# Kernel tuning notes

Hardware: AMD Instinct MI355X
Metric: run time of the kernel (lower is better)

Reference implementation:

```python
import jax, jax.numpy as jnp
import numpy as np

B, N, E, DIN, DOUT = 8, 4096, 1024, 256, 256
EPS = 1e-8

def setup_inputs() -> dict:
    key = jax.random.key(0)
    k1, k2, k3, k4 = jax.random.split(key, 4)
    x = jax.random.normal(k1, (B, N, DIN), dtype=jnp.float32)
    H = jax.random.uniform(k2, (B, N, E), dtype=jnp.float32)
    weight = jax.random.normal(k3, (DIN, DOUT), dtype=jnp.float32) * (1.0 / np.sqrt(DOUT))
    bias = jax.random.normal(k4, (DOUT,), dtype=jnp.float32) * (1.0 / np.sqrt(DOUT))
    return {"x": x, "hypergraph_matrix": H, "weight": weight, "bias": bias}

def reference(x, hypergraph_matrix, weight, bias):
    H = hypergraph_matrix                      # [B, N, E]
    d_v = jnp.clip(jnp.sum(H, axis=2), EPS)    # node degrees [B, N]
    d_v_inv_sqrt = d_v ** -0.5
    d_e = jnp.clip(jnp.sum(H, axis=1), EPS)    # hyperedge degrees [B, E]
    d_e_inv = 1.0 / d_e
    # D_v^{-1/2} H D_e^{-1}
    step2 = d_v_inv_sqrt[:, :, None] * H * d_e_inv[:, None, :]   # [B, N, E]
    # (D_v^{-1/2} H D_e^{-1} H^T) D_v^{-1/2}  -- original materializes [B, N, N]
    step3 = jnp.einsum('bne,bme->bnm', step2, H)                 # [B, N, N]
    normalized_matrix = step3 * d_v_inv_sqrt[:, None, :]         # [B, N, N]
    support = jnp.einsum('bnd,df->bnf', x, weight)               # X Theta
    out = jnp.einsum('bnm,bmf->bnf', normalized_matrix, support) + bias
    # dropout is identity in eval / deterministic baseline
    return out
```

## Files before the change

### kernel.cpp

```cpp
#include <hip/hip_runtime.h>
#include <hip/hip_bf16.h>

#define BATCH 8
#define NN 4096
#define EE 1024
#define DIN 256
#define DOUT 256
#define EPS 1e-8f

typedef short bf16x8 __attribute__((ext_vector_type(8)));
typedef float f32x4 __attribute__((ext_vector_type(4)));

__device__ __forceinline__ unsigned short f2bf(float f) {
    unsigned u = __float_as_uint(f);
    return (unsigned short)((u + 0x7FFFu + ((u >> 16) & 1u)) >> 16);
}

__device__ __forceinline__ void g2l16(const void* g, void* l) {
    __builtin_amdgcn_global_load_lds(
        (const __attribute__((address_space(1))) unsigned*)g,
        (__attribute__((address_space(3))) unsigned*)l, 16, 0, 0);
}


template <int LD>
__device__ __forceinline__ void stage_tile(const unsigned short* src, int k0, short* lds, int tid) {
#pragma unroll
    for (int j = 0; j < 2; ++j) {
        int q = tid + j * 256;
        int r = q >> 2;
        int c = (q ^ (r >> 1)) & 3;
        g2l16(src + (size_t)r * LD + k0 + c * 8, (char*)lds + q * 16);
    }
}

__device__ __forceinline__ bf16x8 frag_ld(const short* lds, int r, int c) {
    int off = (r << 6) | (((c ^ (r >> 1)) & 3) << 4);
    return *(const bf16x8*)((const char*)lds + off);
}

template <int LDA, int LDB>
__device__ __forceinline__ void gemm_core(const unsigned short* A, const unsigned short* B,
                                          int kIters, int k0, f32x4 acc[4][4],
                                          short* As, short* Bs) {
    int tid = threadIdx.x, lane = tid & 63, wave = tid >> 6;
    int wm = (wave >> 1) * 64, wn = (wave & 1) * 64;
    int fr = lane & 15, fc = lane >> 4;
    for (int kt = 0; kt < kIters; ++kt) {
        int k = k0 + kt * 32;
        __syncthreads();
        stage_tile<LDA>(A, k, As, tid);
        stage_tile<LDB>(B, k, Bs, tid);
        __syncthreads();
        bf16x8 av[4], bv[4];
#pragma unroll
        for (int i = 0; i < 4; ++i) av[i] = frag_ld(As, wm + i * 16 + fr, fc);
#pragma unroll
        for (int j = 0; j < 4; ++j) bv[j] = frag_ld(Bs, wn + j * 16 + fr, fc);
#pragma unroll
        for (int i = 0; i < 4; ++i)
#pragma unroll
            for (int j = 0; j < 4; ++j)
                acc[i][j] = __builtin_amdgcn_mfma_f32_16x16x32_bf16(av[i], bv[j], acc[i][j], 0, 0, 0);
    }
}


__global__ __launch_bounds__(256) void prep_h(const float* __restrict__ H,
                                              unsigned short* __restrict__ Hb,
                                              unsigned short* __restrict__ Ht,
                                              float* __restrict__ dv_acc,
                                              float* __restrict__ de_acc) {
    __shared__ float tile[64][65];
    int bid = blockIdx.x;
    int b = bid >> 10;
    int nt = (bid >> 4) & 63, et = bid & 15;
    int n0 = nt * 64, e0 = et * 64;
    int t = threadIdx.x;
    int r = t >> 2, cq = (t & 3) * 16;
    const float* src = H + ((size_t)(b * NN + n0 + r)) * EE + e0 + cq;
    float v[16];
    float rs = 0.f;
#pragma unroll
    for (int j = 0; j < 16; j += 4) {
        float4 x4 = *(const float4*)(src + j);
        v[j] = x4.x; v[j + 1] = x4.y; v[j + 2] = x4.z; v[j + 3] = x4.w;
        rs += x4.x + x4.y + x4.z + x4.w;
    }
    bf16x8 p0, p1;
#pragma unroll
    for (int j = 0; j < 8; ++j) { p0[j] = (short)f2bf(v[j]); p1[j] = (short)f2bf(v[8 + j]); }
    unsigned short* hd = Hb + ((size_t)(b * NN + n0 + r)) * EE + e0 + cq;
    *(bf16x8*)hd = p0; *(bf16x8*)(hd + 8) = p1;
    rs += __shfl_down(rs, 2);
    rs += __shfl_down(rs, 1);
    if ((t & 3) == 0) atomicAdd(dv_acc + b * NN + n0 + r, rs);
#pragma unroll
    for (int j = 0; j < 16; ++j) tile[r][cq + j] = v[j];
    __syncthreads();
    int c = t >> 2, rq = (t & 3) * 16;
    float cs = 0.f;
    bf16x8 q0, q1;
#pragma unroll
    for (int j = 0; j < 16; ++j) {
        float x = tile[rq + j][c];
        cs += x;
        if (j < 8) q0[j] = (short)f2bf(x); else q1[j - 8] = (short)f2bf(x);
    }
    cs += __shfl_down(cs, 2);
    cs += __shfl_down(cs, 1);
    if ((t & 3) == 0) atomicAdd(de_acc + b * EE + e0 + c, cs);
    unsigned short* td = Ht + ((size_t)(b * EE + e0 + c)) * NN + n0 + rq;
    *(bf16x8*)td = q0; *(bf16x8*)(td + 8) = q1;
}

__global__ __launch_bounds__(256) void prep_xw(const float* __restrict__ X,
                                               const float* __restrict__ W,
                                               unsigned short* __restrict__ Xb,
                                               unsigned short* __restrict__ Wt) {
    __shared__ float tile[64][65];
    int bid = blockIdx.x;
    int t = threadIdx.x;
    if (bid < 2048) {
        size_t base = ((size_t)bid * 256 + t) * 16;
        bf16x8 p0, p1;
#pragma unroll
        for (int j = 0; j < 16; j += 4) {
            float4 x4 = *(const float4*)(X + base + j);
            unsigned short a = f2bf(x4.x), b2 = f2bf(x4.y), c2 = f2bf(x4.z), d2 = f2bf(x4.w);
            if (j < 8) { p0[j] = (short)a; p0[j+1] = (short)b2; p0[j+2] = (short)c2; p0[j+3] = (short)d2; }
            else       { p1[j-8] = (short)a; p1[j-7] = (short)b2; p1[j-6] = (short)c2; p1[j-5] = (short)d2; }
        }
        *(bf16x8*)(Xb + base) = p0; *(bf16x8*)(Xb + base + 8) = p1;
    } else {
        int w = bid - 2048;
        int k0 = (w >> 2) * 64, f0 = (w & 3) * 64;
        int r = t >> 2, cq = (t & 3) * 16;
#pragma unroll
        for (int j = 0; j < 16; j += 4) {
            float4 x4 = *(const float4*)(W + (size_t)(k0 + r) * DOUT + f0 + cq + j);
            tile[r][cq + j] = x4.x; tile[r][cq + j + 1] = x4.y;
            tile[r][cq + j + 2] = x4.z; tile[r][cq + j + 3] = x4.w;
        }
        __syncthreads();
        int c = t >> 2, rq = (t & 3) * 16;
        bf16x8 q0, q1;
#pragma unroll
        for (int j = 0; j < 16; ++j) {
            float x = tile[rq + j][c];
            if (j < 8) q0[j] = (short)f2bf(x); else q1[j - 8] = (short)f2bf(x);
        }
        unsigned short* dst = Wt + (size_t)(f0 + c) * DIN + k0 + rq;
        *(bf16x8*)dst = q0; *(bf16x8*)(dst + 8) = q1;
    }
}


__global__ __launch_bounds__(256) void mfma_xw(const unsigned short* __restrict__ Xb,
                                               const unsigned short* __restrict__ Wt,
                                               const float* __restrict__ dv_acc,
                                               unsigned short* __restrict__ Tt) {
    __shared__ short As[128 * 32], Bs[128 * 32];
    int m0 = blockIdx.x * 128, f0 = blockIdx.y * 128;
    f32x4 acc[4][4] = {};
    gemm_core<DIN, DIN>(Xb + (size_t)m0 * DIN, Wt + (size_t)f0 * DIN, DIN / 32, 0, acc, As, Bs);
    int lane = threadIdx.x & 63, wave = threadIdx.x >> 6;
    int wm = (wave >> 1) * 64, wn = (wave & 1) * 64;
    int rg = (lane >> 4) * 4, cl = lane & 15;
    int b = m0 >> 12, nb = m0 & (NN - 1);
#pragma unroll
    for (int i = 0; i < 4; ++i) {
        int rbase = wm + i * 16 + rg;
        float4 dv = *(const float4*)(dv_acc + m0 + rbase);
        float s0 = rsqrtf(fmaxf(dv.x, EPS)), s1 = rsqrtf(fmaxf(dv.y, EPS));
        float s2 = rsqrtf(fmaxf(dv.z, EPS)), s3 = rsqrtf(fmaxf(dv.w, EPS));
#pragma unroll
        for (int j = 0; j < 4; ++j) {
            int f = f0 + wn + j * 16 + cl;
            f32x4 a = acc[i][j];
            ushort4 o = { f2bf(a.x * s0), f2bf(a.y * s1), f2bf(a.z * s2), f2bf(a.w * s3) };
            *(ushort4*)(Tt + (((size_t)b * DOUT + f) << 12) + nb + rbase) = o;
        }
    }
}

__global__ __launch_bounds__(256) void mfma_ht(const unsigned short* __restrict__ Ht,
                                               const unsigned short* __restrict__ Tt,
                                               float* __restrict__ P) {
    __shared__ short As[128 * 32], Bs[128 * 32];
    int e0 = blockIdx.x * 128, f0 = blockIdx.y * 128;
    int b = blockIdx.z >> 2, s = blockIdx.z & 3;
    f32x4 acc[4][4] = {};
    gemm_core<NN, NN>(Ht + ((size_t)b * EE + e0) * NN, Tt + ((size_t)b * DOUT + f0) * NN,
                      1024 / 32, s * 1024, acc, As, Bs);
    int lane = threadIdx.x & 63, wave = threadIdx.x >> 6;
    int wm = (wave >> 1) * 64, wn = (wave & 1) * 64;
    int rg = (lane >> 4) * 4, cl = lane & 15;
    float* Pb = P + (size_t)s * (BATCH * DOUT * EE) + (size_t)b * (DOUT * EE);
#pragma unroll
    for (int i = 0; i < 4; ++i) {
        int e = e0 + wm + i * 16 + rg;
#pragma unroll
        for (int j = 0; j < 4; ++j) {
            int f = f0 + wn + j * 16 + cl;
            *(f32x4*)(Pb + (size_t)f * EE + e) = acc[i][j];
        }
    }
}

__global__ __launch_bounds__(256) void combine_u(const float* __restrict__ P,
                                                 const float* __restrict__ de_acc,
                                                 unsigned short* __restrict__ Ut) {
    const int PS = BATCH * DOUT * EE;
    int idx = (blockIdx.x * 256 + threadIdx.x) * 4;
    f32x4 s = *(const f32x4*)(P + idx);
    s += *(const f32x4*)(P + PS + idx);
    s += *(const f32x4*)(P + 2 * PS + idx);
    s += *(const f32x4*)(P + 3 * PS + idx);
    int b = idx >> 18, e = idx & (EE - 1);
    float4 de = *(const float4*)(de_acc + b * EE + e);
    ushort4 o = { f2bf(s.x / fmaxf(de.x, EPS)), f2bf(s.y / fmaxf(de.y, EPS)),
                  f2bf(s.z / fmaxf(de.z, EPS)), f2bf(s.w / fmaxf(de.w, EPS)) };
    *(ushort4*)(Ut + idx) = o;
}

__global__ __launch_bounds__(256) void mfma_hu(const unsigned short* __restrict__ Ut,
                                               const unsigned short* __restrict__ Hb,
                                               const float* __restrict__ dv_acc,
                                               const float* __restrict__ bias,
                                               float* __restrict__ out) {
    __shared__ short As[128 * 32], Bs[128 * 32];
    int f0 = blockIdx.x * 128, n0 = blockIdx.y * 128, b = blockIdx.z;
    f32x4 acc[4][4] = {};
    gemm_core<EE, EE>(Ut + ((size_t)b * DOUT + f0) * EE, Hb + ((size_t)b * NN + n0) * EE,
                      EE / 32, 0, acc, As, Bs);
    int lane = threadIdx.x & 63, wave = threadIdx.x >> 6;
    int wm = (wave >> 1) * 64, wn = (wave & 1) * 64;
    int rg = (lane >> 4) * 4, cl = lane & 15;
    float dvv[4];
#pragma unroll
    for (int j = 0; j < 4; ++j) {
        int n = n0 + wn + j * 16 + cl;
        dvv[j] = rsqrtf(fmaxf(dv_acc[b * NN + n], EPS));
    }
#pragma unroll
    for (int i = 0; i < 4; ++i) {
        int f = f0 + wm + i * 16 + rg;
        float4 bi = *(const float4*)(bias + f);
#pragma unroll
        for (int j = 0; j < 4; ++j) {
            int n = n0 + wn + j * 16 + cl;
            f32x4 a = acc[i][j];
            float4 o = { a.x * dvv[j] + bi.x, a.y * dvv[j] + bi.y,
                         a.z * dvv[j] + bi.z, a.w * dvv[j] + bi.w };
            *(float4*)(out + (((size_t)b * NN + n) << 8) + f) = o;
        }
    }
}


__global__ __launch_bounds__(256) void dv_kernel(const float* __restrict__ H, float* __restrict__ dv_is) {
    int row = blockIdx.x * 4 + (threadIdx.x >> 6);
    int lane = threadIdx.x & 63;
    const float4* p = (const float4*)(H + (size_t)row * EE);
    float s = 0.f;
#pragma unroll
    for (int j = 0; j < 4; ++j) { float4 v = p[j * 64 + lane]; s += v.x + v.y + v.z + v.w; }
#pragma unroll
    for (int off = 32; off; off >>= 1) s += __shfl_down(s, off);
    if (lane == 0) dv_is[row] = rsqrtf(fmaxf(s, EPS));
}
__global__ void zero_kernel(float* __restrict__ p, int n) {
    int i = blockIdx.x * 256 + threadIdx.x;
    if (i < n) p[i] = 0.f;
}
__global__ __launch_bounds__(256) void de_kernel(const float* __restrict__ H, float* __restrict__ de_acc) {
    int b = blockIdx.x >> 4, chunk = blockIdx.x & 15;
    int e = blockIdx.y * 256 + threadIdx.x;
    const float* p = H + ((size_t)b * NN + chunk * 256) * EE + e;
    float s = 0.f;
    for (int n = 0; n < 256; ++n) s += p[(size_t)n * EE];
    atomicAdd(&de_acc[b * EE + e], s);
}
__global__ void de_finalize(float* __restrict__ de) {
    int i = blockIdx.x * 256 + threadIdx.x;
    de[i] = 1.0f / fmaxf(de[i], EPS);
}
__global__ __launch_bounds__(256) void gemm_xw(const float* __restrict__ X, const float* __restrict__ W,
                                               const float* __restrict__ dv_is, float* __restrict__ T) {
    int b = blockIdx.z;
    int m0 = blockIdx.x * 64, f0 = blockIdx.y * 64;
    const float* A = X + (size_t)b * NN * DIN;
    __shared__ float As[16][68];
    __shared__ float Bs[16][68];
    int tid = threadIdx.x;
    int ar = tid >> 2, ac = (tid & 3) << 2;
    int br = tid >> 4, bc = (tid & 15) << 2;
    int r0 = (tid >> 4) << 2, c0 = (tid & 15) << 2;
    float acc[4][4] = {};
    for (int k0 = 0; k0 < DIN; k0 += 16) {
        float4 av = *(const float4*)&A[(size_t)(m0 + ar) * DIN + k0 + ac];
        float4 bv = *(const float4*)&W[(size_t)(k0 + br) * DOUT + f0 + bc];
        __syncthreads();
        As[ac + 0][ar] = av.x; As[ac + 1][ar] = av.y; As[ac + 2][ar] = av.z; As[ac + 3][ar] = av.w;
        *(float4*)&Bs[br][bc] = bv;
        __syncthreads();
#pragma unroll
        for (int k = 0; k < 16; ++k) {
            float4 a4 = *(const float4*)&As[k][r0];
            float4 b4 = *(const float4*)&Bs[k][c0];
            float a[4] = {a4.x, a4.y, a4.z, a4.w};
            float bb[4] = {b4.x, b4.y, b4.z, b4.w};
#pragma unroll
            for (int i = 0; i < 4; ++i)
#pragma unroll
                for (int j = 0; j < 4; ++j) acc[i][j] = fmaf(a[i], bb[j], acc[i][j]);
        }
    }
#pragma unroll
    for (int i = 0; i < 4; ++i) {
        float dv = dv_is[b * NN + m0 + r0 + i];
        float4 o = {dv * acc[i][0], dv * acc[i][1], dv * acc[i][2], dv * acc[i][3]};
        *(float4*)&T[((size_t)b * NN + m0 + r0 + i) * DOUT + f0 + c0] = o;
    }
}
__global__ __launch_bounds__(256) void gemm_ht(const float* __restrict__ H, const float* __restrict__ T,
                                               const float* __restrict__ de_inv, float* __restrict__ U) {
    int b = blockIdx.z;
    int e0 = blockIdx.x * 64, f0 = blockIdx.y * 64;
    const float* Hb = H + (size_t)b * NN * EE;
    const float* Tb = T + (size_t)b * NN * DOUT;
    __shared__ float As[16][68];
    __shared__ float Bs[16][68];
    int tid = threadIdx.x;
    int lr = tid >> 4, lc = (tid & 15) << 2;
    int r0 = (tid >> 4) << 2, c0 = (tid & 15) << 2;
    float acc[4][4] = {};
    for (int n0 = 0; n0 < NN; n0 += 16) {
        float4 av = *(const float4*)&Hb[(size_t)(n0 + lr) * EE + e0 + lc];
        float4 bv = *(const float4*)&Tb[(size_t)(n0 + lr) * DOUT + f0 + lc];
        __syncthreads();
        *(float4*)&As[lr][lc] = av;
        *(float4*)&Bs[lr][lc] = bv;
        __syncthreads();
#pragma unroll
        for (int k = 0; k < 16; ++k) {
            float4 a4 = *(const float4*)&As[k][r0];
            float4 b4 = *(const float4*)&Bs[k][c0];
            float a[4] = {a4.x, a4.y, a4.z, a4.w};
            float bb[4] = {b4.x, b4.y, b4.z, b4.w};
#pragma unroll
            for (int i = 0; i < 4; ++i)
#pragma unroll
                for (int j = 0; j < 4; ++j) acc[i][j] = fmaf(a[i], bb[j], acc[i][j]);
        }
    }
#pragma unroll
    for (int i = 0; i < 4; ++i) {
        float de = de_inv[b * EE + e0 + r0 + i];
        float4 o = {de * acc[i][0], de * acc[i][1], de * acc[i][2], de * acc[i][3]};
        *(float4*)&U[((size_t)b * EE + e0 + r0 + i) * DOUT + f0 + c0] = o;
    }
}
__global__ __launch_bounds__(256) void gemm_hu(const float* __restrict__ H, const float* __restrict__ U,
                                               const float* __restrict__ dv_is, const float* __restrict__ bias,
                                               float* __restrict__ out) {
    int b = blockIdx.z;
    int n0 = blockIdx.x * 64, f0 = blockIdx.y * 64;
    const float* Hb = H + (size_t)b * NN * EE;
    const float* Ub = U + (size_t)b * EE * DOUT;
    __shared__ float As[16][68];
    __shared__ float Bs[16][68];
    int tid = threadIdx.x;
    int ar = tid >> 2, ac = (tid & 3) << 2;
    int br = tid >> 4, bc = (tid & 15) << 2;
    int r0 = (tid >> 4) << 2, c0 = (tid & 15) << 2;
    float acc[4][4] = {};
    for (int k0 = 0; k0 < EE; k0 += 16) {
        float4 av = *(const float4*)&Hb[(size_t)(n0 + ar) * EE + k0 + ac];
        float4 bv = *(const float4*)&Ub[(size_t)(k0 + br) * DOUT + f0 + bc];
        __syncthreads();
        As[ac + 0][ar] = av.x; As[ac + 1][ar] = av.y; As[ac + 2][ar] = av.z; As[ac + 3][ar] = av.w;
        *(float4*)&Bs[br][bc] = bv;
        __syncthreads();
#pragma unroll
        for (int k = 0; k < 16; ++k) {
            float4 a4 = *(const float4*)&As[k][r0];
            float4 b4 = *(const float4*)&Bs[k][c0];
            float a[4] = {a4.x, a4.y, a4.z, a4.w};
            float bb[4] = {b4.x, b4.y, b4.z, b4.w};
#pragma unroll
            for (int i = 0; i < 4; ++i)
#pragma unroll
                for (int j = 0; j < 4; ++j) acc[i][j] = fmaf(a[i], bb[j], acc[i][j]);
        }
    }
    float4 bi = *(const float4*)&bias[f0 + c0];
#pragma unroll
    for (int i = 0; i < 4; ++i) {
        float dv = dv_is[b * NN + n0 + r0 + i];
        float4 o = {dv * acc[i][0] + bi.x, dv * acc[i][1] + bi.y, dv * acc[i][2] + bi.z, dv * acc[i][3] + bi.w};
        *(float4*)&out[((size_t)b * NN + n0 + r0 + i) * DOUT + f0 + c0] = o;
    }
}

extern "C" void kernel_launch(void* const* d_in, const int* in_sizes, int n_in,
                              void* d_out, int out_size, void* d_ws, size_t ws_size,
                              hipStream_t stream) {
    const float* x    = (const float*)d_in[0];
    const float* H    = (const float*)d_in[1];
    const float* W    = (const float*)d_in[2];
    const float* bias = (const float*)d_in[3];
    float* out = (float*)d_out;

    const size_t NEED = (size_t)(BATCH * NN + BATCH * EE + 4 * BATCH * DOUT * EE) * 4 +
                        (size_t)(DIN * DOUT + BATCH * DOUT * EE +
                                 (size_t)BATCH * NN * EE * 2) * 2;

    if (ws_size >= NEED) {
        float* dv_acc = (float*)d_ws;
        float* de_acc = dv_acc + BATCH * NN;
        float* P      = de_acc + BATCH * EE;
        unsigned short* Wt = (unsigned short*)(P + (size_t)4 * BATCH * DOUT * EE);
        unsigned short* Ut = Wt + DIN * DOUT;
        unsigned short* Hb = Ut + (size_t)BATCH * DOUT * EE;
        unsigned short* Ht = Hb + (size_t)BATCH * NN * EE;
        unsigned short* Xb = (unsigned short*)d_out;
        unsigned short* Tt = Xb + (size_t)BATCH * NN * DOUT;

        hipMemsetAsync(dv_acc, 0, (size_t)(BATCH * NN + BATCH * EE) * sizeof(float), stream);
        prep_h<<<8192, 256, 0, stream>>>(H, Hb, Ht, dv_acc, de_acc);
        prep_xw<<<2064, 256, 0, stream>>>(x, W, Xb, Wt);
        mfma_xw<<<dim3(256, 2), 256, 0, stream>>>(Xb, Wt, dv_acc, Tt);
        mfma_ht<<<dim3(8, 2, 32), 256, 0, stream>>>(Ht, Tt, P);
        combine_u<<<2048, 256, 0, stream>>>(P, de_acc, Ut);
        mfma_hu<<<dim3(2, 32, 8), 256, 0, stream>>>(Ut, Hb, dv_acc, bias, out);
    } else {
        float* ws = (float*)d_ws;
        float* dv_is = ws;
        float* de    = ws + BATCH * NN;
        float* U     = de + BATCH * EE;
        float* T = out;
        dv_kernel<<<BATCH * NN / 4, 256, 0, stream>>>(H, dv_is);
        zero_kernel<<<(BATCH * EE + 255) / 256, 256, 0, stream>>>(de, BATCH * EE);
        de_kernel<<<dim3(BATCH * 16, EE / 256), 256, 0, stream>>>(H, de);
        de_finalize<<<BATCH * EE / 256, 256, 0, stream>>>(de);
        gemm_xw<<<dim3(NN / 64, DOUT / 64, BATCH), 256, 0, stream>>>(x, W, dv_is, T);
        gemm_ht<<<dim3(EE / 64, DOUT / 64, BATCH), 256, 0, stream>>>(H, T, de, U);
        gemm_hu<<<dim3(NN / 64, DOUT / 64, BATCH), 256, 0, stream>>>(H, U, dv_is, bias, out);
    }
}
```

Baseline: 351.6 us.

## Drop row-major bf16 H copy; convert fp32 H inline in final GEMM

The prep kernel no longer writes a row-major bf16 copy of H and now emits only the transposed bf16 copy plus degree sums. Each block loops over 512 rows, which lets it accumulate hyperedge degrees locally and issue fewer atomics. The final GEMM reads fp32 H directly and converts it to bf16 while staging into LDS, removing a 64 MB write and an extra pass. In exchange the final GEMM reads twice as many bytes of H, and its B-tile load becomes synchronous rather than an async global-to-LDS copy. Packed bf16 conversion intrinsics also replace the manual rounding.

```diff
diff --git a/kernel.cpp b/kernel.cpp
--- a/kernel.cpp
+++ b/kernel.cpp
@@ -14,6 +14,17 @@
 __device__ __forceinline__ unsigned short f2bf(float f) {
     unsigned u = __float_as_uint(f);
     return (unsigned short)((u + 0x7FFFu + ((u >> 16) & 1u)) >> 16);
+}
+
+__device__ __forceinline__ unsigned pk2(float lo, float hi) {
+    __hip_bfloat162 h = __float22bfloat162_rn(float2{lo, hi});
+    return *(unsigned*)&h;
+}
+__device__ __forceinline__ bf16x8 pack8(float4 a, float4 b) {
+    union { bf16x8 v; unsigned u[4]; } r;
+    r.u[0] = pk2(a.x, a.y); r.u[1] = pk2(a.z, a.w);
+    r.u[2] = pk2(b.x, b.y); r.u[3] = pk2(b.z, b.w);
+    return r.v;
 }
 
 __device__ __forceinline__ void g2l16(const void* g, void* l) {
@@ -66,52 +77,46 @@
 }
 
 
-__global__ __launch_bounds__(256) void prep_h(const float* __restrict__ H,
-                                              unsigned short* __restrict__ Hb,
-                                              unsigned short* __restrict__ Ht,
-                                              float* __restrict__ dv_acc,
-                                              float* __restrict__ de_acc) {
+__global__ __launch_bounds__(256) void prep_tr(const float* __restrict__ H,
+                                               unsigned short* __restrict__ Ht,
+                                               float* __restrict__ dv_acc,
+                                               float* __restrict__ de_acc) {
     __shared__ float tile[64][65];
-    int bid = blockIdx.x;
-    int b = bid >> 10;
-    int nt = (bid >> 4) & 63, et = bid & 15;
-    int n0 = nt * 64, e0 = et * 64;
+    int ns = blockIdx.x, et = blockIdx.y, b = blockIdx.z;
+    int e0 = et * 64;
     int t = threadIdx.x;
     int r = t >> 2, cq = (t & 3) * 16;
-    const float* src = H + ((size_t)(b * NN + n0 + r)) * EE + e0 + cq;
-    float v[16];
-    float rs = 0.f;
-#pragma unroll
-    for (int j = 0; j < 16; j += 4) {
-        float4 x4 = *(const float4*)(src + j);
-        v[j] = x4.x; v[j + 1] = x4.y; v[j + 2] = x4.z; v[j + 3] = x4.w;
-        rs += x4.x + x4.y + x4.z + x4.w;
-    }
-    bf16x8 p0, p1;
-#pragma unroll
-    for (int j = 0; j < 8; ++j) { p0[j] = (short)f2bf(v[j]); p1[j] = (short)f2bf(v[8 + j]); }
-    unsigned short* hd = Hb + ((size_t)(b * NN + n0 + r)) * EE + e0 + cq;
-    *(bf16x8*)hd = p0; *(bf16x8*)(hd + 8) = p1;
-    rs += __shfl_down(rs, 2);
-    rs += __shfl_down(rs, 1);
-    if ((t & 3) == 0) atomicAdd(dv_acc + b * NN + n0 + r, rs);
-#pragma unroll
-    for (int j = 0; j < 16; ++j) tile[r][cq + j] = v[j];
-    __syncthreads();
-    int c = t >> 2, rq = (t & 3) * 16;
-    float cs = 0.f;
-    bf16x8 q0, q1;
-#pragma unroll
-    for (int j = 0; j < 16; ++j) {
-        float x = tile[rq + j][c];
-        cs += x;
-        if (j < 8) q0[j] = (short)f2bf(x); else q1[j - 8] = (short)f2bf(x);
-    }
-    cs += __shfl_down(cs, 2);
-    cs += __shfl_down(cs, 1);
-    if ((t & 3) == 0) atomicAdd(de_acc + b * EE + e0 + c, cs);
-    unsigned short* td = Ht + ((size_t)(b * EE + e0 + c)) * NN + n0 + rq;
-    *(bf16x8*)td = q0; *(bf16x8*)(td + 8) = q1;
+    int c = t >> 2, q = (t & 3) * 16;
+    float de_part = 0.f;
+    for (int it = 0; it < 8; ++it) {
+        int n0 = ns * 512 + it * 64;
+        const float* src = H + ((size_t)(b * NN + n0 + r)) * EE + e0 + cq;
+        float4 v0 = *(const float4*)(src + 0);
+        float4 v1 = *(const float4*)(src + 4);
+        float4 v2 = *(const float4*)(src + 8);
+        float4 v3 = *(const float4*)(src + 12);
+        float rs = v0.x + v0.y + v0.z + v0.w + v1.x + v1.y + v1.z + v1.w +
+                   v2.x + v2.y + v2.z + v2.w + v3.x + v3.y + v3.z + v3.w;
+        rs += __shfl_down(rs, 2);
+        rs += __shfl_down(rs, 1);
+        __syncthreads();
+        tile[cq + 0][r] = v0.x;  tile[cq + 1][r] = v0.y;  tile[cq + 2][r] = v0.z;  tile[cq + 3][r] = v0.w;
+        tile[cq + 4][r] = v1.x;  tile[cq + 5][r] = v1.y;  tile[cq + 6][r] = v1.z;  tile[cq + 7][r] = v1.w;
+        tile[cq + 8][r] = v2.x;  tile[cq + 9][r] = v2.y;  tile[cq + 10][r] = v2.z; tile[cq + 11][r] = v2.w;
+        tile[cq + 12][r] = v3.x; tile[cq + 13][r] = v3.y; tile[cq + 14][r] = v3.z; tile[cq + 15][r] = v3.w;
+        if ((t & 3) == 0) atomicAdd(dv_acc + b * NN + n0 + r, rs);
+        __syncthreads();
+        float w[16];
+#pragma unroll
+        for (int j = 0; j < 16; ++j) { w[j] = tile[c][q + j]; de_part += w[j]; }
+        bf16x8 p0 = pack8(float4{w[0], w[1], w[2], w[3]}, float4{w[4], w[5], w[6], w[7]});
+        bf16x8 p1 = pack8(float4{w[8], w[9], w[10], w[11]}, float4{w[12], w[13], w[14], w[15]});
+        unsigned short* dst = Ht + ((size_t)(b * EE + e0 + c)) * NN + n0 + q;
+        *(bf16x8*)dst = p0; *(bf16x8*)(dst + 8) = p1;
+    }
+    de_part += __shfl_down(de_part, 2);
+    de_part += __shfl_down(de_part, 1);
+    if ((t & 3) == 0) atomicAdd(de_acc + b * EE + e0 + c, de_part);
 }
 
 __global__ __launch_bounds__(256) void prep_xw(const float* __restrict__ X,
@@ -123,15 +128,12 @@
     int t = threadIdx.x;
     if (bid < 2048) {
         size_t base = ((size_t)bid * 256 + t) * 16;
-        bf16x8 p0, p1;
-#pragma unroll
-        for (int j = 0; j < 16; j += 4) {
-            float4 x4 = *(const float4*)(X + base + j);
-            unsigned short a = f2bf(x4.x), b2 = f2bf(x4.y), c2 = f2bf(x4.z), d2 = f2bf(x4.w);
-            if (j < 8) { p0[j] = (short)a; p0[j+1] = (short)b2; p0[j+2] = (short)c2; p0[j+3] = (short)d2; }
-            else       { p1[j-8] = (short)a; p1[j-7] = (short)b2; p1[j-6] = (short)c2; p1[j-5] = (short)d2; }
-        }
-        *(bf16x8*)(Xb + base) = p0; *(bf16x8*)(Xb + base + 8) = p1;
+        float4 a0 = *(const float4*)(X + base + 0);
+        float4 a1 = *(const float4*)(X + base + 4);
+        float4 a2 = *(const float4*)(X + base + 8);
+        float4 a3 = *(const float4*)(X + base + 12);
+        *(bf16x8*)(Xb + base) = pack8(a0, a1);
+        *(bf16x8*)(Xb + base + 8) = pack8(a2, a3);
     } else {
         int w = bid - 2048;
         int k0 = (w >> 2) * 64, f0 = (w & 3) * 64;
@@ -225,17 +227,44 @@
 }
 
 __global__ __launch_bounds__(256) void mfma_hu(const unsigned short* __restrict__ Ut,
-                                               const unsigned short* __restrict__ Hb,
+                                               const float* __restrict__ Hf,
                                                const float* __restrict__ dv_acc,
                                                const float* __restrict__ bias,
                                                float* __restrict__ out) {
     __shared__ short As[128 * 32], Bs[128 * 32];
     int f0 = blockIdx.x * 128, n0 = blockIdx.y * 128, b = blockIdx.z;
+    const unsigned short* A = Ut + ((size_t)b * DOUT + f0) * EE;
+    const float* Bsrc = Hf + ((size_t)(b * NN + n0)) * EE;
+    int tid = threadIdx.x, lane = tid & 63, wave = tid >> 6;
+    int wm = (wave >> 1) * 64, wn = (wave & 1) * 64;
+    int fr = lane & 15, fc = lane >> 4;
+    int br = tid >> 1, bh = tid & 1;
     f32x4 acc[4][4] = {};
-    gemm_core<EE, EE>(Ut + ((size_t)b * DOUT + f0) * EE, Hb + ((size_t)b * NN + n0) * EE,
-                      EE / 32, 0, acc, As, Bs);
-    int lane = threadIdx.x & 63, wave = threadIdx.x >> 6;
-    int wm = (wave >> 1) * 64, wn = (wave & 1) * 64;
+    for (int kt = 0; kt < EE / 32; ++kt) {
+        int k = kt * 32;
+        __syncthreads();
+        stage_tile<EE>(A, k, As, tid);
+        const float* s = Bsrc + (size_t)br * EE + k + bh * 16;
+        float4 x0 = *(const float4*)(s + 0);
+        float4 x1 = *(const float4*)(s + 4);
+        float4 x2 = *(const float4*)(s + 8);
+        float4 x3 = *(const float4*)(s + 12);
+        bf16x8 p0 = pack8(x0, x1), p1 = pack8(x2, x3);
+        int c0 = 2 * bh, c1 = 2 * bh + 1;
+        *(bf16x8*)((char*)Bs + (br << 6) + (((c0 ^ (br >> 1)) & 3) << 4)) = p0;
+        *(bf16x8*)((char*)Bs + (br << 6) + (((c1 ^ (br >> 1)) & 3) << 4)) = p1;
+        __syncthreads();
+        bf16x8 av[4], bv[4];
+#pragma unroll
+        for (int i = 0; i < 4; ++i) av[i] = frag_ld(As, wm + i * 16 + fr, fc);
+#pragma unroll
+        for (int j = 0; j < 4; ++j) bv[j] = frag_ld(Bs, wn + j * 16 + fr, fc);
+#pragma unroll
+        for (int i = 0; i < 4; ++i)
+#pragma unroll
+            for (int j = 0; j < 4; ++j)
+                acc[i][j] = __builtin_amdgcn_mfma_f32_16x16x32_bf16(av[i], bv[j], acc[i][j], 0, 0, 0);
+    }
     int rg = (lane >> 4) * 4, cl = lane & 15;
     float dvv[4];
 #pragma unroll
@@ -414,8 +443,7 @@
     float* out = (float*)d_out;
 
     const size_t NEED = (size_t)(BATCH * NN + BATCH * EE + 4 * BATCH * DOUT * EE) * 4 +
-                        (size_t)(DIN * DOUT + BATCH * DOUT * EE +
-                                 (size_t)BATCH * NN * EE * 2) * 2;
+                        (size_t)(DIN * DOUT + BATCH * DOUT * EE + (size_t)BATCH * NN * EE) * 2;
 
     if (ws_size >= NEED) {
         float* dv_acc = (float*)d_ws;
@@ -423,18 +451,17 @@
         float* P      = de_acc + BATCH * EE;
         unsigned short* Wt = (unsigned short*)(P + (size_t)4 * BATCH * DOUT * EE);
         unsigned short* Ut = Wt + DIN * DOUT;
-        unsigned short* Hb = Ut + (size_t)BATCH * DOUT * EE;
-        unsigned short* Ht = Hb + (size_t)BATCH * NN * EE;
+        unsigned short* Ht = Ut + (size_t)BATCH * DOUT * EE;
         unsigned short* Xb = (unsigned short*)d_out;
         unsigned short* Tt = Xb + (size_t)BATCH * NN * DOUT;
 
         hipMemsetAsync(dv_acc, 0, (size_t)(BATCH * NN + BATCH * EE) * sizeof(float), stream);
-        prep_h<<<8192, 256, 0, stream>>>(H, Hb, Ht, dv_acc, de_acc);
+        prep_tr<<<dim3(8, 16, 8), 256, 0, stream>>>(H, Ht, dv_acc, de_acc);
         prep_xw<<<2064, 256, 0, stream>>>(x, W, Xb, Wt);
         mfma_xw<<<dim3(256, 2), 256, 0, stream>>>(Xb, Wt, dv_acc, Tt);
         mfma_ht<<<dim3(8, 2, 32), 256, 0, stream>>>(Ht, Tt, P);
         combine_u<<<2048, 256, 0, stream>>>(P, de_acc, Ut);
-        mfma_hu<<<dim3(2, 32, 8), 256, 0, stream>>>(Ut, Hb, dv_acc, bias, out);
+        mfma_hu<<<dim3(2, 32, 8), 256, 0, stream>>>(Ut, H, dv_acc, bias, out);
     } else {
         float* ws = (float*)d_ws;
         float* dv_is = ws;
```

Measured after the change: 357.9 us. No clear change (+1.8%).
